# Kernel tuning notes

Measured on AMD Instinct MI355X. Metric: run time of the kernel, lower is better.

Reference implementation:

```python
import jax, jax.numpy as jnp
import numpy as np

NMAX = 1
MARGIN = 0.2
N, D = 16384, 256

def setup_inputs() -> dict:
    key = jax.random.key(0)
    k1, k2 = jax.random.split(key)
    imgs = jax.random.normal(k1, (N, D), dtype=jnp.float32)
    caps = jax.random.normal(k2, (N, D), dtype=jnp.float32)
    return {"imgs": imgs, "caps": caps}

def reference(imgs, caps):
    # scores[i, j] = <img_i, cap_j>
    scores = imgs @ caps.T                      # [N, N]
    diag = jnp.diagonal(scores)                 # [N]
    s = scores - 2.0 * jnp.diag(diag)
    # hardest negatives per caption (top over image axis = rows) -> [nmax, N]
    max_c = jax.lax.top_k(s.T, NMAX)[0].T
    # hardest negatives per image (top over caption axis = cols) -> [N, nmax]
    max_i = jax.lax.top_k(s, NMAX)[0]
    neg_cap = jnp.sum(jnp.maximum(max_c + (MARGIN - diag)[None, :], 0.0))
    neg_img = jnp.sum(jnp.maximum(max_i + (MARGIN - diag)[:, None], 0.0))
    return neg_cap + neg_img
```

## Files before the change

### kernel.cpp

```cpp
#include <hip/hip_runtime.h>
#include <hip/hip_bf16.h>
#include <hip/hip_fp8.h>
#include <stdint.h>
#include <math.h>

#define NN 16384
#define DD 256
#define MARGIN_F 0.2f

typedef __attribute__((ext_vector_type(8))) int int32x8;
typedef __attribute__((ext_vector_type(4))) float f32x4;

__device__ inline unsigned fkey(float f) {
    unsigned b = __float_as_uint(f);
    return (b & 0x80000000u) ? ~b : (b | 0x80000000u);
}
__device__ inline float fdec(unsigned k) {
    return __uint_as_float((k & 0x80000000u) ? (k ^ 0x80000000u) : ~k);
}
#define NEG_INF_KEY 0x007FFFFFu

__device__ inline void gload16(const void* g, void* l) {
    __builtin_amdgcn_global_load_lds(
        (const __attribute__((address_space(1))) void*)g,
        (__attribute__((address_space(3))) void*)l, 16, 0, 0);
}

__device__ inline unsigned pk8(float4 v) {
    __hip_fp8_e4m3 q0(v.x), q1(v.y), q2(v.z), q3(v.w);
    return (unsigned)q0.__x | ((unsigned)q1.__x << 8) |
           ((unsigned)q2.__x << 16) | ((unsigned)q3.__x << 24);
}

__global__ __launch_bounds__(256) void fused_prep_kernel(
    const float* __restrict__ imgs, const float* __restrict__ caps,
    unsigned char* __restrict__ imgs8, unsigned char* __restrict__ caps8,
    float* __restrict__ diag, unsigned* __restrict__ rowmax,
    unsigned* __restrict__ colmax) {
    const int i = (blockIdx.x << 2) + (threadIdx.x >> 6);
    const int l = threadIdx.x & 63;
    const float4* a4 = reinterpret_cast<const float4*>(imgs + (size_t)i * DD);
    const float4* b4 = reinterpret_cast<const float4*>(caps + (size_t)i * DD);
    float4 av = a4[l];
    float4 bv = b4[l];
    reinterpret_cast<unsigned*>(imgs8 + (size_t)i * DD)[l] = pk8(av);
    reinterpret_cast<unsigned*>(caps8 + (size_t)i * DD)[l] = pk8(bv);
    float s = av.x * bv.x + av.y * bv.y + av.z * bv.z + av.w * bv.w;
    #pragma unroll
    for (int off = 32; off > 0; off >>= 1) s += __shfl_down(s, off);
    if (l == 0) {
        diag[i] = s;
        rowmax[i] = NEG_INF_KEY;
        colmax[i] = NEG_INF_KEY;
    }
}

__global__ __launch_bounds__(256, 2) void score_max_kernel(
    const unsigned char* __restrict__ imgs8,
    const unsigned char* __restrict__ caps8,
    const float* __restrict__ diag,
    unsigned* __restrict__ rowmax, unsigned* __restrict__ colmax) {

    __shared__ char lds[49152];
    float* clds = reinterpret_cast<float*>(lds + 32768);

    const int bid   = blockIdx.x;
    const int panel = bid >> 2;
    const int strip = bid & 3;
    const int brow  = panel << 7;
    const int scol  = strip << 12;

    const int t    = threadIdx.x;
    const int wid  = t >> 6;
    const int lane = t & 63;
    const int rg   = lane >> 4;
    const int cl   = lane & 15;

    #pragma unroll
    for (int i = 0; i < 16; ++i) clds[t + (i << 8)] = -INFINITY;

    const int sl = t & 15;
    const int rw = t >> 4;
    const int srcoff = (((sl >> 1) ^ (rw & 7)) << 5) + ((sl & 1) << 4);

    {
        const unsigned char* src =
            imgs8 + (((size_t)(brow + rw)) << 8) + srcoff;
        #pragma unroll
        for (int i = 0; i < 8; ++i)
            gload16(src + ((size_t)i << 12), lds + t * 16 + i * 4096);
    }
    __syncthreads();

    int32x8 af[8][2];
    #pragma unroll
    for (int m = 0; m < 8; ++m) {
        const int row = m * 16 + cl;
        #pragma unroll
        for (int ks = 0; ks < 2; ++ks)
            af[m][ks] = *reinterpret_cast<const int32x8*>(
                lds + row * 256 + (((rg + (ks << 2)) ^ (cl & 7)) << 5));
    }
    __syncthreads();

    #define STAGEB(bo, cb) {                                                   \
        const unsigned char* s_ =                                              \
            caps8 + (((size_t)((cb) + rw)) << 8) + srcoff;                     \
        _Pragma("unroll")                                                      \
        for (int i_ = 0; i_ < 4; ++i_)                                         \
            gload16(s_ + ((size_t)i_ << 12), lds + (bo) + t * 16 + i_ * 4096); \
    }

    STAGEB(0, scol);

    float rmx[8][4];
    #pragma unroll
    for (int m = 0; m < 8; ++m)
        #pragma unroll
        for (int r = 0; r < 4; ++r) rmx[m][r] = -INFINITY;

    const int rr = (wid << 4) + cl;
    unsigned boff[2];
    #pragma unroll
    for (int ks = 0; ks < 2; ++ks)
        boff[ks] = rr * 256 + (((rg + (ks << 2)) ^ (cl & 7)) << 5);

    const f32x4 zv = (f32x4){0.f, 0.f, 0.f, 0.f};
    #define SCL 0x7F7F7F7F

    for (int h = 0; h < 64; ++h) {
        const int cb = scol + (h << 6);
        const int bo = (h & 1) << 14;

        __builtin_amdgcn_s_barrier();
        asm volatile("" ::: "memory");
        if (h < 63) {
            STAGEB(bo ^ 16384, cb + 64);
            asm volatile("s_waitcnt vmcnt(4)" ::: "memory");
        } else {
            asm volatile("s_waitcnt vmcnt(0)" ::: "memory");
        }
        __builtin_amdgcn_s_barrier();
        asm volatile("" ::: "memory");

        const char* buf = lds + bo;
        int32x8 b0 = *reinterpret_cast<const int32x8*>(buf + boff[0]);
        int32x8 b1 = *reinterpret_cast<const int32x8*>(buf + boff[1]);

        f32x4 acc[8];
        __builtin_amdgcn_s_setprio(1);
        #pragma unroll
        for (int m = 0; m < 8; ++m)
            acc[m] = __builtin_amdgcn_mfma_scale_f32_16x16x128_f8f6f4(
                af[m][0], b0, zv, 0, 0, 0, SCL, 0, SCL);
        #pragma unroll
        for (int m = 0; m < 8; ++m)
            acc[m] = __builtin_amdgcn_mfma_scale_f32_16x16x128_f8f6f4(
                af[m][1], b1, acc[m], 0, 0, 0, SCL, 0, SCL);
        __builtin_amdgcn_s_setprio(0);

        const int cfb = cb + (wid << 4);
        if (cfb < brow + 128 && cfb + 16 > brow) {
            #pragma unroll
            for (int m = 0; m < 8; ++m)
                #pragma unroll
                for (int r = 0; r < 4; ++r) {
                    const int gi = brow + m * 16 + (rg << 2) + r;
                    if (gi - cfb == cl) acc[m][r] = -diag[gi];
                }
        }

        #pragma unroll
        for (int m = 0; m < 8; ++m)
            #pragma unroll
            for (int r = 0; r < 4; ++r)
                rmx[m][r] = fmaxf(rmx[m][r], acc[m][r]);

        {
            float v = fmaxf(fmaxf(acc[0][0], acc[0][1]),
                            fmaxf(acc[0][2], acc[0][3]));
            #pragma unroll
            for (int m = 1; m < 8; ++m)
                v = fmaxf(v, fmaxf(fmaxf(acc[m][0], acc[m][1]),
                                   fmaxf(acc[m][2], acc[m][3])));
            v = fmaxf(v, __shfl_xor(v, 16));
            v = fmaxf(v, __shfl_xor(v, 32));
            if (rg == 0) {
                const int c = cfb + cl - scol;
                clds[c] = fmaxf(clds[c], v);
            }
        }
    }

    #pragma unroll
    for (int m = 0; m < 8; ++m)
        #pragma unroll
        for (int r = 0; r < 4; ++r) {
            float v = rmx[m][r];
            v = fmaxf(v, __shfl_xor(v, 1));
            v = fmaxf(v, __shfl_xor(v, 2));
            v = fmaxf(v, __shfl_xor(v, 4));
            v = fmaxf(v, __shfl_xor(v, 8));
            if (cl == 0)
                atomicMax(&rowmax[brow + m * 16 + (rg << 2) + r], fkey(v));
        }

    __syncthreads();
    #pragma unroll
    for (int i = 0; i < 16; ++i) {
        const int c = t + (i << 8);
        atomicMax(&colmax[scol + c], fkey(clds[c]));
    }
    #undef STAGEB
}

__global__ __launch_bounds__(1024) void finalize_kernel(
    const float* __restrict__ diag,
    const unsigned* __restrict__ rowmax,
    const unsigned* __restrict__ colmax,
    float* __restrict__ out) {
    __shared__ float red[1024];
    int t = threadIdx.x;
    float s = 0.f;
    for (int idx = t; idx < 2 * NN; idx += 1024) {
        int i = idx & (NN - 1);
        float mx = fdec((idx < NN) ? colmax[i] : rowmax[i]);
        s += fmaxf(mx + (MARGIN_F - diag[i]), 0.f);
    }
    red[t] = s;
    __syncthreads();
    for (int off = 512; off > 0; off >>= 1) {
        if (t < off) red[t] += red[t + off];
        __syncthreads();
    }
    if (t == 0) out[0] = red[0];
}

extern "C" void kernel_launch(void* const* d_in, const int* in_sizes, int n_in,
                              void* d_out, int out_size, void* d_ws, size_t ws_size,
                              hipStream_t stream) {
    const float* imgs = reinterpret_cast<const float*>(d_in[0]);
    const float* caps = reinterpret_cast<const float*>(d_in[1]);

    float* diag          = reinterpret_cast<float*>(d_ws);
    unsigned* rowmax     = reinterpret_cast<unsigned*>(diag + NN);
    unsigned* colmax     = rowmax + NN;
    unsigned char* imgs8 = reinterpret_cast<unsigned char*>(colmax + NN);
    unsigned char* caps8 = imgs8 + (size_t)NN * DD;

    fused_prep_kernel<<<NN / 4, 256, 0, stream>>>(imgs, caps, imgs8, caps8,
                                                  diag, rowmax, colmax);

    score_max_kernel<<<512, 256, 0, stream>>>(imgs8, caps8, diag,
                                              rowmax, colmax);

    finalize_kernel<<<1, 1024, 0, stream>>>(diag, rowmax, colmax,
                                            reinterpret_cast<float*>(d_out));
}
```

Before: 108.2 us.

## Load caption fragments directly from global into registers, drop LDS double buffer

Replaces the LDS double-buffered staging of caption tiles, with its two barriers per iteration, by per-wave direct global loads into registers, prefetching the next tile's fragments one iteration ahead. Each wave loads only its own 16 columns, so there is no data sharing across waves and all block-wide synchronization in the main loop goes away. The cost is uncoalesced 32-byte global loads per lane and global latency that a single iteration of MFMA work may not hide.

New measurement: 95.16 us. -12.0%, faster.

```diff
diff --git a/kernel.cpp b/kernel.cpp
--- a/kernel.cpp
+++ b/kernel.cpp
@@ -79,11 +79,10 @@
     #pragma unroll
     for (int i = 0; i < 16; ++i) clds[t + (i << 8)] = -INFINITY;
 
-    const int sl = t & 15;
-    const int rw = t >> 4;
-    const int srcoff = (((sl >> 1) ^ (rw & 7)) << 5) + ((sl & 1) << 4);
-
     {
+        const int sl = t & 15;
+        const int rw = t >> 4;
+        const int srcoff = (((sl >> 1) ^ (rw & 7)) << 5) + ((sl & 1) << 4);
         const unsigned char* src =
             imgs8 + (((size_t)(brow + rw)) << 8) + srcoff;
         #pragma unroll
@@ -101,17 +100,6 @@
             af[m][ks] = *reinterpret_cast<const int32x8*>(
                 lds + row * 256 + (((rg + (ks << 2)) ^ (cl & 7)) << 5));
     }
-    __syncthreads();
-
-    #define STAGEB(bo, cb) {                                                   \
-        const unsigned char* s_ =                                              \
-            caps8 + (((size_t)((cb) + rw)) << 8) + srcoff;                     \
-        _Pragma("unroll")                                                      \
-        for (int i_ = 0; i_ < 4; ++i_)                                         \
-            gload16(s_ + ((size_t)i_ << 12), lds + (bo) + t * 16 + i_ * 4096); \
-    }
-
-    STAGEB(0, scol);
 
     float rmx[8][4];
     #pragma unroll
@@ -119,33 +107,22 @@
         #pragma unroll
         for (int r = 0; r < 4; ++r) rmx[m][r] = -INFINITY;
 
-    const int rr = (wid << 4) + cl;
-    unsigned boff[2];
-    #pragma unroll
-    for (int ks = 0; ks < 2; ++ks)
-        boff[ks] = rr * 256 + (((rg + (ks << 2)) ^ (cl & 7)) << 5);
+    const unsigned char* pb =
+        caps8 + (((size_t)(scol + (wid << 4) + cl)) << 8) + (rg << 5);
 
     const f32x4 zv = (f32x4){0.f, 0.f, 0.f, 0.f};
     #define SCL 0x7F7F7F7F
 
+    int32x8 b0 = *reinterpret_cast<const int32x8*>(pb);
+    int32x8 b1 = *reinterpret_cast<const int32x8*>(pb + 128);
+
     for (int h = 0; h < 64; ++h) {
         const int cb = scol + (h << 6);
-        const int bo = (h & 1) << 14;
-
-        __builtin_amdgcn_s_barrier();
-        asm volatile("" ::: "memory");
-        if (h < 63) {
-            STAGEB(bo ^ 16384, cb + 64);
-            asm volatile("s_waitcnt vmcnt(4)" ::: "memory");
-        } else {
-            asm volatile("s_waitcnt vmcnt(0)" ::: "memory");
-        }
-        __builtin_amdgcn_s_barrier();
-        asm volatile("" ::: "memory");
-
-        const char* buf = lds + bo;
-        int32x8 b0 = *reinterpret_cast<const int32x8*>(buf + boff[0]);
-        int32x8 b1 = *reinterpret_cast<const int32x8*>(buf + boff[1]);
+        const int hn = (h < 63) ? h + 1 : h;
+        const unsigned char* pn = pb + ((size_t)hn << 14);
+
+        int32x8 bn0 = *reinterpret_cast<const int32x8*>(pn);
+        int32x8 bn1 = *reinterpret_cast<const int32x8*>(pn + 128);
 
         f32x4 acc[8];
         __builtin_amdgcn_s_setprio(1);
@@ -190,6 +167,9 @@
                 clds[c] = fmaxf(clds[c], v);
             }
         }
+
+        b0 = bn0;
+        b1 = bn1;
     }
 
     #pragma unroll
@@ -211,7 +191,6 @@
         const int c = t + (i << 8);
         atomicMax(&colmax[scol + c], fkey(clds[c]));
     }
-    #undef STAGEB
 }
 
 __global__ __launch_bounds__(1024) void finalize_kernel(
```
